# Optimization experiments

Measured on AMD Instinct MI355X. Metric: run time of the kernel, lower is better.

The kernel has to match this reference:

```python
import jax, jax.numpy as jnp
import numpy as np

N, E, IN, H, C, OUT = 100000, 800000, 256, 4, 32, 64
NEG_SLOPE = 0.2


def _glorot(key, shape):
    fan = shape[0] if len(shape) > 1 else shape[-1]
    return jax.random.normal(key, shape, dtype=jnp.float32) * (1.0 / np.sqrt(fan))


def setup_inputs() -> dict:
    key = jax.random.key(0)
    ks = jax.random.split(key, 24)
    inp = {
        'x': jax.random.normal(ks[0], (N, IN), dtype=jnp.float32),
        'edge_index': jax.random.randint(ks[1], (2, E), 0, N, dtype=jnp.int64),
        # GATConv layer 0: 256 -> 4 heads x 32 (concat -> 128)
        'W0': _glorot(ks[2], (IN, H * C)), 'b0': jnp.zeros((H * C,), jnp.float32),
        'as0': _glorot(ks[3], (H, C)), 'ad0': _glorot(ks[4], (H, C)),
        # GATConv layer 1: 128 -> 4 heads x 32 (concat -> 128)
        'W1': _glorot(ks[5], (H * C, H * C)), 'b1': jnp.zeros((H * C,), jnp.float32),
        'as1': _glorot(ks[6], (H, C)), 'ad1': _glorot(ks[7], (H, C)),
        # GATConv layer 2: 128 -> 1 head x 64 (mean, concat=False)
        'W2': _glorot(ks[8], (H * C, OUT)), 'b2': jnp.zeros((OUT,), jnp.float32),
        'as2': _glorot(ks[9], (1, OUT)), 'ad2': _glorot(ks[10], (1, OUT)),
        # skip projections: layer0 Linear(256->128), layer1 Identity, layer2 Linear(128->64)
        'skip0_W': _glorot(ks[11], (IN, H * C)), 'skip0_b': jnp.zeros((H * C,), jnp.float32),
        'skip2_W': _glorot(ks[12], (H * C, OUT)), 'skip2_b': jnp.zeros((OUT,), jnp.float32),
        # JK concat linear: (128+128+64) -> 64
        'jk_W': _glorot(ks[13], (2 * H * C + OUT, OUT)), 'jk_b': jnp.zeros((OUT,), jnp.float32),
    }
    return inp


def gat_layer(x, src, dst, n, W, b, a_src, a_dst, heads, concat):
    # x: [N, F_in]; src/dst: [E'] (self-loops included); W: [F_in, heads*C]
    xh = (x @ W).reshape(n, heads, -1)                    # [N, H, C]
    al_src = jnp.einsum('nhc,hc->nh', xh, a_src)          # [N, H]
    al_dst = jnp.einsum('nhc,hc->nh', xh, a_dst)
    e = jax.nn.leaky_relu(al_src[src] + al_dst[dst], NEG_SLOPE)   # [E', H]
    emax = jax.ops.segment_max(e, dst, num_segments=n)    # self-loops => every segment nonempty
    w = jnp.exp(e - emax[dst])                            # [E', H]
    denom = jax.ops.segment_sum(w, dst, num_segments=n)   # [N, H]
    msg = xh[src] * w[:, :, None]                         # [E', H, C]
    out = jax.ops.segment_sum(msg, dst, num_segments=n) / denom[:, :, None]
    if concat:
        return out.reshape(n, -1) + b
    return out.mean(axis=1) + b


def reference(x, edge_index, W0, b0, as0, ad0, W1, b1, as1, ad1, W2, b2, as2, ad2,
              skip0_W, skip0_b, skip2_W, skip2_b, jk_W, jk_b):
    n = x.shape[0]
    loops = jnp.arange(n, dtype=edge_index.dtype)
    src = jnp.concatenate([edge_index[0], loops])
    dst = jnp.concatenate([edge_index[1], loops])
    # layer 0 (dropout is identity in eval mode)
    res0 = x @ skip0_W + skip0_b
    h = gat_layer(x, src, dst, n, W0, b0, as0, ad0, H, True) + res0
    h = jax.nn.elu(h)
    x0 = h
    # layer 1 (skip proj is Identity: 128 == 128)
    h = gat_layer(h, src, dst, n, W1, b1, as1, ad1, H, True) + h
    h = jax.nn.elu(h)
    x1 = h
    # layer 2 (1 head, concat=False -> head mean; no ELU)
    res2 = h @ skip2_W + skip2_b
    h = gat_layer(h, src, dst, n, W2, b2, as2, ad2, 1, False) + res2
    # JumpingKnowledge 'cat' + linear
    jk = jnp.concatenate([x0, x1, h], axis=-1)            # [N, 320]
    return jk @ jk_W + jk_b                               # [N, 64]
```

## Files before the change

kernel.cpp:

```cpp
#include <hip/hip_runtime.h>
#include <hip/hip_bf16.h>
#include <cstdint>

static constexpr int NN = 100000;
static constexpr int NE = 800000;
static constexpr int EP = NE + NN;
static constexpr int NB = (NN + 255) / 256;

typedef unsigned short ushort;
typedef __attribute__((ext_vector_type(8))) short short8;
typedef __attribute__((ext_vector_type(8))) ushort ushort8v;
typedef __attribute__((ext_vector_type(4))) float f32x4;

__device__ __forceinline__ float leaky(float x) { return x > 0.f ? x : 0.2f * x; }

__device__ __forceinline__ ushort f2bf(float f) {
    unsigned int u = __float_as_uint(f);
    u += 0x7fffu + ((u >> 16) & 1u);
    return (ushort)(u >> 16);
}
__device__ __forceinline__ float bf2f(ushort h) {
    return __uint_as_float(((unsigned int)h) << 16);
}

__device__ __forceinline__ void gload16(const void* g, void* l) {
    __builtin_amdgcn_global_load_lds((__attribute__((address_space(1))) void*)g,
                                     (__attribute__((address_space(3))) void*)l,
                                     16, 0, 0);
}

__device__ __forceinline__ void waitbar4() {
    asm volatile("s_waitcnt vmcnt(4)" ::: "memory");
    __builtin_amdgcn_s_barrier();
    __builtin_amdgcn_sched_barrier(0);
}

__global__ void pretile_kernel(const float* __restrict__ Wa, const float* __restrict__ Wb,
                               int K, int CS, int NT,
                               ushort* __restrict__ Whi, ushort* __restrict__ Wlo)
{
    int idx = blockIdx.x * 256 + threadIdx.x;
    if (idx >= K * NT) return;
    int k = idx / NT, c = idx - k * NT;
    float v = (c < CS) ? Wa[(size_t)k * CS + c] : Wb[(size_t)k * (NT - CS) + (c - CS)];
    ushort h = f2bf(v);
    ushort l = f2bf(v - bf2f(h));
    size_t o = ((size_t)(k >> 5) * NT + c) * 32 + (k & 31);
    Whi[o] = h; Wlo[o] = l;
}

template<int KTOT, int NTOT, int NCB, int K1, int K2, int CSPLIT, int BIAS_OFF,
         int AHH, int ACC, int ATTN, bool ASPLIT, bool Y1BF, int MINW>
__global__ __launch_bounds__(256, MINW)
void gemm_mfma(const void* __restrict__ X1, const void* __restrict__ X1b,
               const void* __restrict__ X2, const void* __restrict__ X2b,
               const void* __restrict__ X3, const void* __restrict__ X3b,
               int ldx1, int ldx2, int ldx3,
               const ushort* __restrict__ Wthi, const ushort* __restrict__ Wtlo,
               const float* __restrict__ bias,
               void* __restrict__ Y1, float* __restrict__ Y2, int ldy1, int ldy2,
               float* __restrict__ als, float* __restrict__ ald,
               const float* __restrict__ a_src, const float* __restrict__ a_dst,
               int n)
{
    constexpr int NKT = KTOT / 32;
    constexpr int NF  = NCB / 16;

    __shared__ ushort Bh[2][NCB * 32], Bl[2][NCB * 32];

    const int t = threadIdx.x, l = t & 63, w = t >> 6;
    const int lc = l & 15, lq = l >> 4;
    const int wrow = blockIdx.x * 128 + w * 32;
    const int cbase = blockIdx.y * NCB;

    f32x4 acc[2][NF];
#pragma unroll
    for (int mf = 0; mf < 2; ++mf)
#pragma unroll
        for (int nf = 0; nf < NF; ++nf)
            acc[mf][nf] = (f32x4){0.f, 0.f, 0.f, 0.f};

    int arow[2], rcl[2];
#pragma unroll
    for (int mf = 0; mf < 2; ++mf) {
        arow[mf] = wrow + mf * 16 + lc;
        rcl[mf]  = arow[mf] < n ? arow[mf] : (n - 1);
    }

    short8 A0h[2], A0l[2], A1h[2], A1l[2];
    float4 F0[2][2], F1[2][2];

    auto loadA = [&](int kt, short8 (&dh)[2], short8 (&dl)[2], float4 (&df)[2][2]) {
        const int k0 = kt * 32;
        const void* xp; const void* xq; int ldx, koff;
        if (k0 < K1)      { xp = X1; xq = X1b; ldx = ldx1; koff = k0; }
        else if (k0 < K2) { xp = X2; xq = X2b; ldx = ldx2; koff = k0 - K1; }
        else              { xp = X3; xq = X3b; ldx = ldx3; koff = k0 - K2; }
        if constexpr (ASPLIT) {
            const ushort* ph = (const ushort*)xp;
            const ushort* pl = (const ushort*)xq;
#pragma unroll
            for (int mf = 0; mf < 2; ++mf) {
                size_t o = (size_t)rcl[mf] * ldx + koff + lq * 8;
                dh[mf] = *(const short8*)&ph[o];
                dl[mf] = *(const short8*)&pl[o];
            }
        } else {
            const float* pf = (const float*)xp;
#pragma unroll
            for (int mf = 0; mf < 2; ++mf) {
                size_t o = (size_t)rcl[mf] * ldx + koff + lq * 8;
                df[mf][0] = *(const float4*)&pf[o];
                df[mf][1] = *(const float4*)&pf[o + 4];
            }
        }
    };

    auto stageB = [&](int kt, int buf) {
        constexpr int UN = NCB * 4;
#pragma unroll
        for (int s = 0; s < UN / 256; ++s) {
            int unit = s * 256 + t;
            int col  = unit & (NCB - 1);
            int kq   = unit / NCB;
            size_t go = ((size_t)kt * NTOT + cbase + col) * 32 + kq * 8;
            gload16(&Wthi[go], &Bh[buf][unit * 8]);
            gload16(&Wtlo[go], &Bl[buf][unit * 8]);
        }
    };

    stageB(0, 0);
    __builtin_amdgcn_sched_barrier(0);
    loadA(0, A0h, A0l, F0);
    waitbar4();

#pragma unroll
    for (int kt = 0; kt < NKT; ++kt) {
        if (kt + 1 < NKT) {
            stageB(kt + 1, (kt + 1) & 1);
            __builtin_amdgcn_sched_barrier(0);
            if (((kt + 1) & 1) == 0) loadA(kt + 1, A0h, A0l, F0);
            else                     loadA(kt + 1, A1h, A1l, F1);
        }

        short8 ah[2], al[2];
        if constexpr (ASPLIT) {
            if ((kt & 1) == 0) { ah[0]=A0h[0]; ah[1]=A0h[1]; al[0]=A0l[0]; al[1]=A0l[1]; }
            else               { ah[0]=A1h[0]; ah[1]=A1h[1]; al[0]=A1l[0]; al[1]=A1l[1]; }
        } else {
            const auto& Fc = (kt & 1) ? F1 : F0;
#pragma unroll
            for (int mf = 0; mf < 2; ++mf) {
                short8 h8, l8;
#pragma unroll
                for (int e = 0; e < 8; ++e) {
                    float f = (e < 4) ? (&Fc[mf][0].x)[e] : (&Fc[mf][1].x)[e - 4];
                    ushort hh = f2bf(f);
                    h8[e] = (short)hh;
                    l8[e] = (short)f2bf(f - bf2f(hh));
                }
                ah[mf] = h8; al[mf] = l8;
            }
        }

        const int cb = kt & 1;
#pragma unroll
        for (int nf = 0; nf < NF; ++nf) {
            int bslot = lq * NCB + nf * 16 + lc;
            short8 bh = *(const short8*)&Bh[cb][bslot * 8];
            short8 bl = *(const short8*)&Bl[cb][bslot * 8];
#pragma unroll
            for (int mf = 0; mf < 2; ++mf) {
                acc[mf][nf] = __builtin_amdgcn_mfma_f32_16x16x32_bf16(ah[mf], bh, acc[mf][nf], 0, 0, 0);
                acc[mf][nf] = __builtin_amdgcn_mfma_f32_16x16x32_bf16(ah[mf], bl, acc[mf][nf], 0, 0, 0);
                acc[mf][nf] = __builtin_amdgcn_mfma_f32_16x16x32_bf16(al[mf], bh, acc[mf][nf], 0, 0, 0);
            }
        }
        if (kt + 1 < NKT) waitbar4();
    }

    if constexpr (AHH > 0) {
        if (cbase == 0) {
            constexpr int FPH = ACC / 16;
            constexpr int NG  = ATTN / ACC;
#pragma unroll
            for (int g = 0; g < NG; ++g) {
#pragma unroll
                for (int mf = 0; mf < 2; ++mf) {
                    float ps[4] = {0.f, 0.f, 0.f, 0.f};
                    float pd[4] = {0.f, 0.f, 0.f, 0.f};
#pragma unroll
                    for (int j = 0; j < FPH; ++j) {
                        int col = g * ACC + j * 16 + lc;
                        float av = a_src[col], dv = a_dst[col];
#pragma unroll
                        for (int r = 0; r < 4; ++r) {
                            ps[r] = fmaf(acc[mf][g * FPH + j][r], av, ps[r]);
                            pd[r] = fmaf(acc[mf][g * FPH + j][r], dv, pd[r]);
                        }
                    }
#pragma unroll
                    for (int off = 1; off < 16; off <<= 1)
#pragma unroll
                        for (int r = 0; r < 4; ++r) {
                            ps[r] += __shfl_xor(ps[r], off);
                            pd[r] += __shfl_xor(pd[r], off);
                        }
                    if (lc == 0) {
#pragma unroll
                        for (int r = 0; r < 4; ++r) {
                            int row = wrow + mf * 16 + lq * 4 + r;
                            if (row < n) {
                                als[(size_t)row * AHH + g] = ps[r];
                                ald[(size_t)row * AHH + g] = pd[r];
                            }
                        }
                    }
                }
            }
        }
    }

#pragma unroll
    for (int mf = 0; mf < 2; ++mf) {
        int rb4 = wrow + mf * 16 + lq * 4;
#pragma unroll
        for (int nf = 0; nf < NF; ++nf) {
            int col = cbase + nf * 16 + lc;
            float bv = 0.f;
            if constexpr (BIAS_OFF < NTOT) {
                if (col >= BIAS_OFF) bv = bias[col - BIAS_OFF];
            }
#pragma unroll
            for (int r = 0; r < 4; ++r) {
                int row = rb4 + r;
                if (row < n) {
                    float v = acc[mf][nf][r] + bv;
                    if (col < CSPLIT) {
                        if constexpr (Y1BF)
                            ((ushort*)Y1)[(size_t)row * ldy1 + col] = f2bf(v);
                        else
                            ((float*)Y1)[(size_t)row * ldy1 + col] = v;
                    } else {
                        Y2[(size_t)row * ldy2 + (col - CSPLIT)] = v;
                    }
                }
            }
        }
    }
}

__global__ void deg_kernel(const int* __restrict__ ei, int* __restrict__ deg)
{
    int t = blockIdx.x * blockDim.x + threadIdx.x;
    if (t < NE) atomicAdd(&deg[ei[NE + t]], 1);
}

__global__ void block_sum_kernel(const int* __restrict__ deg, int* __restrict__ bsum)
{
    int node = blockIdx.x * 256 + threadIdx.x;
    int v = (node < NN) ? deg[node] + 1 : 0;
#pragma unroll
    for (int off = 32; off > 0; off >>= 1) v += __shfl_down(v, off);
    __shared__ int sh[4];
    if ((threadIdx.x & 63) == 0) sh[threadIdx.x >> 6] = v;
    __syncthreads();
    if (threadIdx.x == 0) bsum[blockIdx.x] = sh[0] + sh[1] + sh[2] + sh[3];
}

__global__ void scan_sums_kernel(const int* __restrict__ bsum, int* __restrict__ bsumx,
                                 int* __restrict__ rowptr)
{
    if (threadIdx.x == 0) {
        int run = 0;
        for (int i = 0; i < NB; ++i) { bsumx[i] = run; run += bsum[i]; }
        rowptr[NN] = run;
    }
}

__global__ void scan_blocks_kernel(const int* __restrict__ deg, const int* __restrict__ bsumx,
                                   int* __restrict__ rowptr, int* __restrict__ cursor)
{
    __shared__ int sh[256];
    int node = blockIdx.x * 256 + threadIdx.x;
    int v = (node < NN) ? deg[node] + 1 : 0;
    sh[threadIdx.x] = v;
    __syncthreads();
#pragma unroll
    for (int off = 1; off < 256; off <<= 1) {
        int tv = (threadIdx.x >= off) ? sh[threadIdx.x - off] : 0;
        __syncthreads();
        sh[threadIdx.x] += tv;
        __syncthreads();
    }
    if (node < NN) {
        int excl = bsumx[blockIdx.x] + sh[threadIdx.x] - v;
        rowptr[node] = excl;
        cursor[node] = excl;
    }
}

__global__ void fill_kernel(const int* __restrict__ ei, int* __restrict__ cursor,
                            int* __restrict__ csr_src)
{
    int t = blockIdx.x * blockDim.x + threadIdx.x;
    if (t >= EP) return;
    int s, d;
    if (t < NE) { s = ei[t]; d = ei[NE + t]; }
    else        { s = d = t - NE; }
    int pos = atomicAdd(&cursor[d], 1);
    csr_src[pos] = s;
}

template<int HH>
__global__ __launch_bounds__(256)
void attn_weights_kernel(const int* __restrict__ rowptr, const int* __restrict__ csr_src,
                         const float* __restrict__ als, const float* __restrict__ ald,
                         float* __restrict__ wq, int n)
{
    int node = blockIdx.x * 256 + threadIdx.x;
    if (node >= n) return;
    const int e0 = rowptr[node], e1 = rowptr[node + 1];
    float aldv[HH], m[HH], d[HH];
#pragma unroll
    for (int h = 0; h < HH; ++h) { m[h] = -1e30f; d[h] = 0.f; }
    if constexpr (HH == 4) {
        float4 a = *(const float4*)&ald[(size_t)node * 4];
        aldv[0] = a.x; aldv[1] = a.y; aldv[2] = a.z; aldv[3] = a.w;
    } else {
        aldv[0] = ald[node];
    }
    for (int e = e0; e < e1; ++e) {
        int s = csr_src[e];
        float av[HH];
        if constexpr (HH == 4) {
            float4 a = *(const float4*)&als[(size_t)s * 4];
            av[0] = a.x; av[1] = a.y; av[2] = a.z; av[3] = a.w;
        } else {
            av[0] = als[s];
        }
#pragma unroll
        for (int h = 0; h < HH; ++h) {
            float sc = leaky(av[h] + aldv[h]);
            float nm = fmaxf(m[h], sc);
            d[h] = d[h] * __expf(m[h] - nm) + __expf(sc - nm);
            m[h] = nm;
        }
    }
#pragma unroll
    for (int h = 0; h < HH; ++h) d[h] = 1.f / d[h];
    for (int e = e0; e < e1; ++e) {
        int s = csr_src[e];
        float av[HH];
        if constexpr (HH == 4) {
            float4 a = *(const float4*)&als[(size_t)s * 4];
            av[0] = a.x; av[1] = a.y; av[2] = a.z; av[3] = a.w;
        } else {
            av[0] = als[s];
        }
        float wv[HH];
#pragma unroll
        for (int h = 0; h < HH; ++h)
            wv[h] = __expf(leaky(av[h] + aldv[h]) - m[h]) * d[h];
        if constexpr (HH == 4) {
            float4 o; o.x = wv[0]; o.y = wv[1]; o.z = wv[2]; o.w = wv[3];
            *(float4*)&wq[(size_t)e * 4] = o;
        } else {
            wq[e] = wv[0];
        }
    }
}

template<int HH, int CC, bool DOELU, bool RESSPLIT>
__global__ __launch_bounds__(256)
void spmm_kernel(const int* __restrict__ rowptr, const int* __restrict__ csr_src,
                 const ushort* __restrict__ xh, const float* __restrict__ wq,
                 const float* __restrict__ b,
                 const float* __restrict__ resf,
                 const ushort* __restrict__ resh, const ushort* __restrict__ resl,
                 ushort* __restrict__ outh, ushort* __restrict__ outl, int n)
{
    constexpr int HCL = HH * CC;
    constexpr int CPL = HCL / 64;
    const int l = threadIdx.x & 63;
    const int node = blockIdx.x * 4 + (threadIdx.x >> 6);
    if (node >= n) return;
    const int c = l * CPL;
    const int h = c / CC;
    const int e0 = rowptr[node], e1 = rowptr[node + 1];

    float a0[CPL], a1[CPL];
#pragma unroll
    for (int j = 0; j < CPL; ++j) { a0[j] = 0.f; a1[j] = 0.f; }

    auto gather = [&](int e, float* accv) {
        int s = csr_src[e];
        float w0 = wq[(size_t)e * HH + h];
        if constexpr (CPL == 2) {
            unsigned int uv = *(const unsigned int*)&xh[(size_t)s * HCL + c];
            accv[0] = fmaf(w0, bf2f((ushort)(uv & 0xffffu)), accv[0]);
            accv[1] = fmaf(w0, bf2f((ushort)(uv >> 16)), accv[1]);
        } else {
            accv[0] = fmaf(w0, bf2f(xh[(size_t)s * HCL + c]), accv[0]);
        }
    };

    int e = e0;
    for (; e + 3 < e1; e += 4) {
        gather(e, a0); gather(e + 1, a1);
        gather(e + 2, a0); gather(e + 3, a1);
    }
    for (; e < e1; ++e) gather(e, a0);

#pragma unroll
    for (int j = 0; j < CPL; ++j) {
        size_t idx = (size_t)node * HCL + c + j;
        float rv;
        if constexpr (RESSPLIT) rv = bf2f(resh[idx]) + bf2f(resl[idx]);
        else                    rv = resf[idx];
        float v = a0[j] + a1[j] + b[c + j] + rv;
        if (DOELU) v = v > 0.f ? v : (__expf(v) - 1.f);
        ushort hh = f2bf(v);
        outh[idx] = hh;
        outl[idx] = f2bf(v - bf2f(hh));
    }
}

extern "C" void kernel_launch(void* const* d_in, const int* in_sizes, int n_in,
                              void* d_out, int out_size, void* d_ws, size_t ws_size,
                              hipStream_t stream)
{
    const float* x    = (const float*)d_in[0];
    const int*   ei   = (const int*)d_in[1];
    const float* W0   = (const float*)d_in[2];
    const float* b0   = (const float*)d_in[3];
    const float* as0  = (const float*)d_in[4];
    const float* ad0  = (const float*)d_in[5];
    const float* W1   = (const float*)d_in[6];
    const float* b1   = (const float*)d_in[7];
    const float* as1  = (const float*)d_in[8];
    const float* ad1  = (const float*)d_in[9];
    const float* W2   = (const float*)d_in[10];
    const float* b2   = (const float*)d_in[11];
    const float* as2  = (const float*)d_in[12];
    const float* ad2  = (const float*)d_in[13];
    const float* sk0W = (const float*)d_in[14];
    const float* sk0b = (const float*)d_in[15];
    const float* sk2W = (const float*)d_in[16];
    const float* sk2b = (const float*)d_in[17];
    const float* jkW  = (const float*)d_in[18];
    const float* jkb  = (const float*)d_in[19];
    float* out = (float*)d_out;

    float* ws = (float*)d_ws;
    size_t off = 0;
    float* s_xh  = ws + off; off += (size_t)NN * 128;
    float* s_r0  = ws + off; off += (size_t)NN * 128;
    float* s_als = ws + off; off += (size_t)NN * 4;
    float* s_ald = ws + off; off += (size_t)NN * 4;
    float* f_wq  = ws + off; off += (size_t)EP * 4;
    ushort* s_xhb = (ushort*)s_xh;
    ushort* u_x0h = (ushort*)(ws + off); off += (size_t)NN * 64;
    ushort* u_x0l = (ushort*)(ws + off); off += (size_t)NN * 64;
    ushort* u_x1h = (ushort*)(ws + off); off += (size_t)NN * 64;
    ushort* u_x1l = (ushort*)(ws + off); off += (size_t)NN * 64;
    ushort* u_h2h = (ushort*)(ws + off); off += (size_t)NN * 32;
    ushort* u_h2l = (ushort*)(ws + off); off += (size_t)NN * 32;
    int* i_deg    = (int*)(ws + off); off += NN;
    int* i_rowptr = (int*)(ws + off); off += NN + 1;
    int* i_cursor = (int*)(ws + off); off += NN;
    int* i_csrsrc = (int*)(ws + off); off += EP;
    int* i_bsum   = (int*)(ws + off); off += NB;
    int* i_bsumx  = (int*)(ws + off); off += NB;
    off = (off + 3) & ~(size_t)3;
    ushort* wt0h = (ushort*)(ws + off); off += 32768;
    ushort* wt0l = (ushort*)(ws + off); off += 32768;
    ushort* wt1h = (ushort*)(ws + off); off += 8192;
    ushort* wt1l = (ushort*)(ws + off); off += 8192;
    ushort* wt2h = (ushort*)(ws + off); off += 8192;
    ushort* wt2l = (ushort*)(ws + off); off += 8192;
    ushort* wtjh = (ushort*)(ws + off); off += 10240;
    ushort* wtjl = (ushort*)(ws + off); off += 10240;

    const int G128 = (NN + 127) / 128;
    const int GN = (NN + 255) / 256;
    const int GS = (NN + 3) / 4;
    constexpr int BIG = 1 << 30;

    hipMemsetAsync(i_deg, 0, (size_t)NN * sizeof(int), stream);
    deg_kernel<<<(NE + 255) / 256, 256, 0, stream>>>(ei, i_deg);
    block_sum_kernel<<<NB, 256, 0, stream>>>(i_deg, i_bsum);
    scan_sums_kernel<<<1, 64, 0, stream>>>(i_bsum, i_bsumx, i_rowptr);
    scan_blocks_kernel<<<NB, 256, 0, stream>>>(i_deg, i_bsumx, i_rowptr, i_cursor);
    fill_kernel<<<(EP + 255) / 256, 256, 0, stream>>>(ei, i_cursor, i_csrsrc);

    pretile_kernel<<<256, 256, 0, stream>>>(W0, sk0W, 256, 128, 256, wt0h, wt0l);
    pretile_kernel<<<64,  256, 0, stream>>>(W1, nullptr, 128, 128, 128, wt1h, wt1l);
    pretile_kernel<<<64,  256, 0, stream>>>(W2, sk2W, 128, 64, 128, wt2h, wt2l);
    pretile_kernel<<<80,  256, 0, stream>>>(jkW, nullptr, 320, 64, 64, wtjh, wtjl);

    gemm_mfma<256, 256, 128, 256, 256, 128, 128, 4, 32, 128, false, true, 3>
        <<<dim3(G128, 2), 256, 0, stream>>>(
        x, nullptr, nullptr, nullptr, nullptr, nullptr, 256, 0, 0,
        wt0h, wt0l, sk0b,
        s_xhb, s_r0, 128, 128, s_als, s_ald, as0, ad0, NN);
    attn_weights_kernel<4><<<GN, 256, 0, stream>>>(
        i_rowptr, i_csrsrc, s_als, s_ald, f_wq, NN);
    spmm_kernel<4, 32, true, false><<<GS, 256, 0, stream>>>(
        i_rowptr, i_csrsrc, s_xhb, f_wq, b0, s_r0, nullptr, nullptr,
        u_x0h, u_x0l, NN);

    gemm_mfma<128, 128, 128, 128, 128, 128, BIG, 4, 32, 128, true, true, 3>
        <<<dim3(G128, 1), 256, 0, stream>>>(
        u_x0h, u_x0l, nullptr, nullptr, nullptr, nullptr, 128, 0, 0,
        wt1h, wt1l, nullptr,
        s_xhb, nullptr, 128, 0, s_als, s_ald, as1, ad1, NN);
    attn_weights_kernel<4><<<GN, 256, 0, stream>>>(
        i_rowptr, i_csrsrc, s_als, s_ald, f_wq, NN);
    spmm_kernel<4, 32, true, true><<<GS, 256, 0, stream>>>(
        i_rowptr, i_csrsrc, s_xhb, f_wq, b1, nullptr, u_x0h, u_x0l,
        u_x1h, u_x1l, NN);

    gemm_mfma<128, 128, 128, 128, 128, 64, 64, 1, 64, 64, true, true, 3>
        <<<dim3(G128, 1), 256, 0, stream>>>(
        u_x1h, u_x1l, nullptr, nullptr, nullptr, nullptr, 128, 0, 0,
        wt2h, wt2l, sk2b,
        s_xhb, s_r0, 64, 64, s_als, s_ald, as2, ad2, NN);
    attn_weights_kernel<1><<<GN, 256, 0, stream>>>(
        i_rowptr, i_csrsrc, s_als, s_ald, f_wq, NN);
    spmm_kernel<1, 64, false, false><<<GS, 256, 0, stream>>>(
        i_rowptr, i_csrsrc, s_xhb, f_wq, b2, s_r0, nullptr, nullptr,
        u_h2h, u_h2l, NN);

    gemm_mfma<320, 64, 64, 128, 256, 64, 0, 0, 16, 0, true, false, 4>
        <<<dim3(G128, 1), 256, 0, stream>>>(
        u_x0h, u_x0l, u_x1h, u_x1l, u_h2h, u_h2l, 128, 128, 64,
        wtjh, wtjl, jkb,
        out, nullptr, 64, 0, nullptr, nullptr, nullptr, nullptr, NN);
}
```

Before: 557.2 us.

## Fuse attention softmax weights into wave-per-node SpMM kernel

Drops the separate per-node attention-weight kernel and the edge-weight buffer it wrote. The SpMM kernel now computes the online-softmax max and denominator itself, with each wave striding over the node's edges and merging partial results through xor shuffles. It then writes per-edge weights into LDS in chunks of 64 edges before gathering features. This removes a global write and read of edge weights and one launch per layer, at the cost of recomputing the source attention scores twice per edge. The layer-0 GEMM is also launched with one column block covering all 256 outputs instead of two, and the last template parameter changes on two GEMMs.

```diff
diff --git a/kernel.cpp b/kernel.cpp
--- a/kernel.cpp
+++ b/kernel.cpp
@@ -312,25 +312,37 @@
     csr_src[pos] = s;
 }
 
-template<int HH>
+template<int HH, int CC, bool DOELU, bool RESSPLIT>
 __global__ __launch_bounds__(256)
-void attn_weights_kernel(const int* __restrict__ rowptr, const int* __restrict__ csr_src,
-                         const float* __restrict__ als, const float* __restrict__ ald,
-                         float* __restrict__ wq, int n)
-{
-    int node = blockIdx.x * 256 + threadIdx.x;
+void spmm_fused_kernel(const int* __restrict__ rowptr, const int* __restrict__ csr_src,
+                       const ushort* __restrict__ xh,
+                       const float* __restrict__ als, const float* __restrict__ ald,
+                       const float* __restrict__ b,
+                       const float* __restrict__ resf,
+                       const ushort* __restrict__ resh, const ushort* __restrict__ resl,
+                       ushort* __restrict__ outh, ushort* __restrict__ outl, int n)
+{
+    constexpr int HCL = HH * CC;
+    constexpr int CPL = HCL / 64;
+    __shared__ float wlds[4][64][HH];
+    const int l = threadIdx.x & 63;
+    const int wv = threadIdx.x >> 6;
+    const int node = blockIdx.x * 4 + wv;
     if (node >= n) return;
+    const int c = l * CPL;
+    const int h = c / CC;
     const int e0 = rowptr[node], e1 = rowptr[node + 1];
+
     float aldv[HH], m[HH], d[HH];
 #pragma unroll
-    for (int h = 0; h < HH; ++h) { m[h] = -1e30f; d[h] = 0.f; }
+    for (int q = 0; q < HH; ++q) { m[q] = -1e30f; d[q] = 0.f; }
     if constexpr (HH == 4) {
         float4 a = *(const float4*)&ald[(size_t)node * 4];
         aldv[0] = a.x; aldv[1] = a.y; aldv[2] = a.z; aldv[3] = a.w;
     } else {
         aldv[0] = ald[node];
     }
-    for (int e = e0; e < e1; ++e) {
+    for (int e = e0 + l; e < e1; e += 64) {
         int s = csr_src[e];
         float av[HH];
         if constexpr (HH == 4) {
@@ -340,62 +352,34 @@
             av[0] = als[s];
         }
 #pragma unroll
-        for (int h = 0; h < HH; ++h) {
-            float sc = leaky(av[h] + aldv[h]);
-            float nm = fmaxf(m[h], sc);
-            d[h] = d[h] * __expf(m[h] - nm) + __expf(sc - nm);
-            m[h] = nm;
-        }
-    }
-#pragma unroll
-    for (int h = 0; h < HH; ++h) d[h] = 1.f / d[h];
-    for (int e = e0; e < e1; ++e) {
+        for (int q = 0; q < HH; ++q) {
+            float sc = leaky(av[q] + aldv[q]);
+            float nm = fmaxf(m[q], sc);
+            d[q] = d[q] * __expf(m[q] - nm) + __expf(sc - nm);
+            m[q] = nm;
+        }
+    }
+#pragma unroll
+    for (int off = 1; off < 64; off <<= 1) {
+#pragma unroll
+        for (int q = 0; q < HH; ++q) {
+            float mo = __shfl_xor(m[q], off);
+            float dn = __shfl_xor(d[q], off);
+            float nm = fmaxf(m[q], mo);
+            d[q] = d[q] * __expf(m[q] - nm) + dn * __expf(mo - nm);
+            m[q] = nm;
+        }
+    }
+    float inv[HH];
+#pragma unroll
+    for (int q = 0; q < HH; ++q) inv[q] = 1.f / d[q];
+
+    float a0[CPL], a1[CPL];
+#pragma unroll
+    for (int j = 0; j < CPL; ++j) { a0[j] = 0.f; a1[j] = 0.f; }
+
+    auto gatherw = [&](int e, float w0, float* accv) {
         int s = csr_src[e];
-        float av[HH];
-        if constexpr (HH == 4) {
-            float4 a = *(const float4*)&als[(size_t)s * 4];
-            av[0] = a.x; av[1] = a.y; av[2] = a.z; av[3] = a.w;
-        } else {
-            av[0] = als[s];
-        }
-        float wv[HH];
-#pragma unroll
-        for (int h = 0; h < HH; ++h)
-            wv[h] = __expf(leaky(av[h] + aldv[h]) - m[h]) * d[h];
-        if constexpr (HH == 4) {
-            float4 o; o.x = wv[0]; o.y = wv[1]; o.z = wv[2]; o.w = wv[3];
-            *(float4*)&wq[(size_t)e * 4] = o;
-        } else {
-            wq[e] = wv[0];
-        }
-    }
-}
-
-template<int HH, int CC, bool DOELU, bool RESSPLIT>
-__global__ __launch_bounds__(256)
-void spmm_kernel(const int* __restrict__ rowptr, const int* __restrict__ csr_src,
-                 const ushort* __restrict__ xh, const float* __restrict__ wq,
-                 const float* __restrict__ b,
-                 const float* __restrict__ resf,
-                 const ushort* __restrict__ resh, const ushort* __restrict__ resl,
-                 ushort* __restrict__ outh, ushort* __restrict__ outl, int n)
-{
-    constexpr int HCL = HH * CC;
-    constexpr int CPL = HCL / 64;
-    const int l = threadIdx.x & 63;
-    const int node = blockIdx.x * 4 + (threadIdx.x >> 6);
-    if (node >= n) return;
-    const int c = l * CPL;
-    const int h = c / CC;
-    const int e0 = rowptr[node], e1 = rowptr[node + 1];
-
-    float a0[CPL], a1[CPL];
-#pragma unroll
-    for (int j = 0; j < CPL; ++j) { a0[j] = 0.f; a1[j] = 0.f; }
-
-    auto gather = [&](int e, float* accv) {
-        int s = csr_src[e];
-        float w0 = wq[(size_t)e * HH + h];
         if constexpr (CPL == 2) {
             unsigned int uv = *(const unsigned int*)&xh[(size_t)s * HCL + c];
             accv[0] = fmaf(w0, bf2f((ushort)(uv & 0xffffu)), accv[0]);
@@ -405,12 +389,31 @@
         }
     };
 
-    int e = e0;
-    for (; e + 3 < e1; e += 4) {
-        gather(e, a0); gather(e + 1, a1);
-        gather(e + 2, a0); gather(e + 3, a1);
-    }
-    for (; e < e1; ++e) gather(e, a0);
+    for (int ebase = e0; ebase < e1; ebase += 64) {
+        int e = ebase + l;
+        if (e < e1) {
+            int s = csr_src[e];
+            float av[HH];
+            if constexpr (HH == 4) {
+                float4 a = *(const float4*)&als[(size_t)s * 4];
+                av[0] = a.x; av[1] = a.y; av[2] = a.z; av[3] = a.w;
+            } else {
+                av[0] = als[s];
+            }
+#pragma unroll
+            for (int q = 0; q < HH; ++q)
+                wlds[wv][l][q] = __expf(leaky(av[q] + aldv[q]) - m[q]) * inv[q];
+        }
+        asm volatile("s_waitcnt lgkmcnt(0)" ::: "memory");
+        int ecnt = (e1 - ebase) < 64 ? (e1 - ebase) : 64;
+        int j = 0;
+        for (; j + 1 < ecnt; j += 2) {
+            gatherw(ebase + j,     wlds[wv][j][h],     a0);
+            gatherw(ebase + j + 1, wlds[wv][j + 1][h], a1);
+        }
+        if (j < ecnt) gatherw(ebase + j, wlds[wv][j][h], a0);
+        asm volatile("" ::: "memory");
+    }
 
 #pragma unroll
     for (int j = 0; j < CPL; ++j) {
@@ -458,7 +461,6 @@
     float* s_r0  = ws + off; off += (size_t)NN * 128;
     float* s_als = ws + off; off += (size_t)NN * 4;
     float* s_ald = ws + off; off += (size_t)NN * 4;
-    float* f_wq  = ws + off; off += (size_t)EP * 4;
     ushort* s_xhb = (ushort*)s_xh;
     ushort* u_x0h = (ushort*)(ws + off); off += (size_t)NN * 64;
     ushort* u_x0l = (ushort*)(ws + off); off += (size_t)NN * 64;
@@ -483,7 +485,6 @@
     ushort* wtjl = (ushort*)(ws + off); off += 10240;
 
     const int G128 = (NN + 127) / 128;
-    const int GN = (NN + 255) / 256;
     const int GS = (NN + 3) / 4;
     constexpr int BIG = 1 << 30;
 
@@ -499,15 +500,13 @@
     pretile_kernel<<<64,  256, 0, stream>>>(W2, sk2W, 128, 64, 128, wt2h, wt2l);
     pretile_kernel<<<80,  256, 0, stream>>>(jkW, nullptr, 320, 64, 64, wtjh, wtjl);
 
-    gemm_mfma<256, 256, 128, 256, 256, 128, 128, 4, 32, 128, false, true, 3>
-        <<<dim3(G128, 2), 256, 0, stream>>>(
+    gemm_mfma<256, 256, 256, 256, 256, 128, 128, 4, 32, 128, false, true, 2>
+        <<<dim3(G128, 1), 256, 0, stream>>>(
         x, nullptr, nullptr, nullptr, nullptr, nullptr, 256, 0, 0,
         wt0h, wt0l, sk0b,
         s_xhb, s_r0, 128, 128, s_als, s_ald, as0, ad0, NN);
-    attn_weights_kernel<4><<<GN, 256, 0, stream>>>(
-        i_rowptr, i_csrsrc, s_als, s_ald, f_wq, NN);
-    spmm_kernel<4, 32, true, false><<<GS, 256, 0, stream>>>(
-        i_rowptr, i_csrsrc, s_xhb, f_wq, b0, s_r0, nullptr, nullptr,
+    spmm_fused_kernel<4, 32, true, false><<<GS, 256, 0, stream>>>(
+        i_rowptr, i_csrsrc, s_xhb, s_als, s_ald, b0, s_r0, nullptr, nullptr,
         u_x0h, u_x0l, NN);
 
     gemm_mfma<128, 128, 128, 128, 128, 128, BIG, 4, 32, 128, true, true, 3>
@@ -515,10 +514,8 @@
         u_x0h, u_x0l, nullptr, nullptr, nullptr, nullptr, 128, 0, 0,
         wt1h, wt1l, nullptr,
         s_xhb, nullptr, 128, 0, s_als, s_ald, as1, ad1, NN);
-    attn_weights_kernel<4><<<GN, 256, 0, stream>>>(
-        i_rowptr, i_csrsrc, s_als, s_ald, f_wq, NN);
-    spmm_kernel<4, 32, true, true><<<GS, 256, 0, stream>>>(
-        i_rowptr, i_csrsrc, s_xhb, f_wq, b1, nullptr, u_x0h, u_x0l,
+    spmm_fused_kernel<4, 32, true, true><<<GS, 256, 0, stream>>>(
+        i_rowptr, i_csrsrc, s_xhb, s_als, s_ald, b1, nullptr, u_x0h, u_x0l,
         u_x1h, u_x1l, NN);
 
     gemm_mfma<128, 128, 128, 128, 128, 64, 64, 1, 64, 64, true, true, 3>
@@ -526,13 +523,11 @@
         u_x1h, u_x1l, nullptr, nullptr, nullptr, nullptr, 128, 0, 0,
         wt2h, wt2l, sk2b,
         s_xhb, s_r0, 64, 64, s_als, s_ald, as2, ad2, NN);
-    attn_weights_kernel<1><<<GN, 256, 0, stream>>>(
-        i_rowptr, i_csrsrc, s_als, s_ald, f_wq, NN);
-    spmm_kernel<1, 64, false, false><<<GS, 256, 0, stream>>>(
-        i_rowptr, i_csrsrc, s_xhb, f_wq, b2, s_r0, nullptr, nullptr,
+    spmm_fused_kernel<1, 64, false, false><<<GS, 256, 0, stream>>>(
+        i_rowptr, i_csrsrc, s_xhb, s_als, s_ald, b2, s_r0, nullptr, nullptr,
         u_h2h, u_h2l, NN);
 
-    gemm_mfma<320, 64, 64, 128, 256, 64, 0, 0, 16, 0, true, false, 4>
+    gemm_mfma<320, 64, 64, 128, 256, 64, 0, 0, 16, 0, true, false, 3>
         <<<dim3(G128, 1), 256, 0, stream>>>(
         u_x0h, u_x0l, u_x1h, u_x1l, u_h2h, u_h2l, 128, 128, 64,
         wtjh, wtjl, jkb,
```

New measurement: 636.6 us. 1.14x slower.
